# Kernel tuning notes

Measured on AMD Instinct MI355X. Metric: run time of the kernel, lower is better.

The kernel has to match this reference:

```python
import math
import jax, jax.numpy as jnp
import numpy as np

DIM = 2048
HEAD_DIM = 64
N_HEADS = DIM // HEAD_DIM
BATCH = 4
SEQ = 1025  # 32*32 axial positions + 1 zero position
EPS = 1e-6


def make_theta(head_dim=HEAD_DIM, h=32, w=32):
    # freqs: geometric from pi to 10*pi, head_dim//4 of them
    n_freqs = head_dim // 4
    freqs = jnp.exp(jnp.linspace(math.log(math.pi), math.log(10 * math.pi), n_freqs))
    hp = jnp.linspace(-1.0, 1.0, h + 1)
    wp = jnp.linspace(-1.0, 1.0, w + 1)
    hp = (hp[:-1] + hp[1:]) / 2
    wp = (wp[:-1] + wp[1:]) / 2
    pos = jnp.stack(jnp.meshgrid(hp, wp, indexing='ij'), axis=-1).reshape(h * w, 2)
    pos = jnp.concatenate([jnp.zeros((1, 2)), pos], axis=0)  # [1025, 2]
    theta_h = pos[:, 0:1] * freqs  # [S, n_freqs]
    theta_w = pos[:, 1:2] * freqs
    return jnp.concatenate([theta_h, theta_w], axis=-1)  # [S, head_dim//2]


def rms_norm(x, scale, eps=EPS):
    mean_sq = jnp.mean(jnp.square(x.astype(jnp.float32)), axis=-1, keepdims=True)
    s = scale.astype(jnp.float32) * jax.lax.rsqrt(mean_sq + eps)
    return (x * s.astype(x.dtype)).astype(x.dtype)


def apply_rotary(x, theta):
    # x: [B, H, S, D], theta: [S, d] with 2*d <= D
    d = theta.shape[-1]
    x1, x2, x3 = x[..., :d], x[..., d:2 * d], x[..., 2 * d:]
    cos, sin = jnp.cos(theta), jnp.sin(theta)  # broadcast over B, H
    y1 = x1 * cos - x2 * sin
    y2 = x2 * cos + x1 * sin
    return jnp.concatenate([y1, y2, x3], axis=-1)


def setup_inputs() -> dict:
    key = jax.random.key(0)
    k1, k2, k3 = jax.random.split(key, 3)
    x = jax.random.normal(k1, (BATCH, SEQ, DIM), dtype=jnp.float32)
    scale = jnp.ones((DIM,), dtype=jnp.float32)
    w_qkv = jax.random.normal(k2, (3 * DIM, DIM), dtype=jnp.float32) * 0.02
    w_out = jax.random.normal(k3, (DIM, DIM), dtype=jnp.float32) * 0.02
    return {"x": x, "scale": scale, "w_qkv": w_qkv, "w_out": w_out}


def reference(x, scale, w_qkv, w_out):
    B, S, _ = x.shape
    skip = x
    h = rms_norm(x, scale)
    qkv = h @ w_qkv.T  # [B, S, 3*DIM]
    qkv = qkv.reshape(B, S, 3, N_HEADS, HEAD_DIM)
    qkv = jnp.transpose(qkv, (0, 3, 2, 1, 4))  # [B, H, 3, S, D]
    q, k, v = qkv[:, :, 0], qkv[:, :, 1], qkv[:, :, 2]
    theta = make_theta()[:S]
    q = apply_rotary(q, theta)
    k = apply_rotary(k, theta)
    scores = jnp.einsum('bhqd,bhkd->bhqk', q, k) / math.sqrt(HEAD_DIM)
    causal = jnp.tril(jnp.ones((S, S), dtype=bool))
    scores = jnp.where(causal, scores, jnp.finfo(scores.dtype).min)
    attn = jax.nn.softmax(scores, axis=-1)
    o = jnp.einsum('bhqk,bhkd->bhqd', attn, v)  # [B, H, S, D]
    o = jnp.transpose(o, (0, 2, 1, 3)).reshape(B, S, DIM)
    return o @ w_out.T + skip
```

## Files before the change

kernel.cpp:

```cpp
#include <hip/hip_runtime.h>
#include <hip/hip_bf16.h>
#include <cstdint>

#define SEQ   1025
#define SPAD  1088
#define DIM   2048
#define NQKV  6144
#define MROWS 4100
#define MPAD  4224
#define NH    32

typedef __attribute__((ext_vector_type(8))) short bf16x8;
typedef __attribute__((ext_vector_type(4))) short bf16x4;
typedef __attribute__((ext_vector_type(4))) float f32x4;

#define MFMA16x16(A,B,C) __builtin_amdgcn_mfma_f32_16x16x32_bf16(A,B,C,0,0,0)

static __device__ __forceinline__ float bf2f(short s) {
    union { unsigned int u; float f; } v;
    v.u = ((unsigned int)(unsigned short)s) << 16;
    return v.f;
}
static __device__ __forceinline__ short f2bf(float f) {
    union { float f; unsigned int u; } v; v.f = f;
    unsigned int r = v.u + 0x7fffu + ((v.u >> 16) & 1u);
    return (short)(r >> 16);
}

typedef __attribute__((address_space(1))) unsigned int u32g;
typedef __attribute__((address_space(3))) unsigned int u32l;
static __device__ __forceinline__ void gld_lds16(void* lds, const void* g) {
    __builtin_amdgcn_global_load_lds((const u32g*)(uintptr_t)g,
                                     (u32l*)(uintptr_t)lds, 16, 0, 0);
}

__global__ __launch_bounds__(256) void trig_k(float* __restrict__ cosT, float* __restrict__ sinT) {
    int i = blockIdx.x * 256 + threadIdx.x;
    if (i >= SEQ * 16) return;
    int s = i >> 4, f = i & 15;
    float ph = 0.f, pw = 0.f;
    if (s > 0) {
        int p = s - 1;
        ph = -1.f + ((p >> 5) + 0.5f) * 0.0625f;
        pw = -1.f + ((p & 31) + 0.5f) * 0.0625f;
    }
    double fr = 3.141592653589793 * exp((double)f * 0.15350567286626973);
    float th = (float)(ph * fr), tw = (float)(pw * fr);
    cosT[s*32 + f]      = cosf(th);
    sinT[s*32 + f]      = sinf(th);
    cosT[s*32 + 16 + f] = cosf(tw);
    sinT[s*32 + 16 + f] = sinf(tw);
}

__global__ __launch_bounds__(256) void rmsnorm_k(const float* __restrict__ x,
                                                 const float* __restrict__ sc,
                                                 short* __restrict__ h) {
    int row = blockIdx.x, t = threadIdx.x;
    short* hr = h + (size_t)row * DIM;
    if (row >= MROWS) {
        bf16x8 z = {};
        *(bf16x8*)(hr + t*8) = z;
        return;
    }
    const float4* xr = (const float4*)(x + (size_t)row * DIM);
    float4 a = xr[2*t], b = xr[2*t+1];
    float ss = a.x*a.x + a.y*a.y + a.z*a.z + a.w*a.w
             + b.x*b.x + b.y*b.y + b.z*b.z + b.w*b.w;
    #pragma unroll
    for (int off = 32; off; off >>= 1) ss += __shfl_xor(ss, off, 64);
    __shared__ float red[4];
    if ((t & 63) == 0) red[t >> 6] = ss;
    __syncthreads();
    float ms = (red[0]+red[1]+red[2]+red[3]) * (1.0f/2048.0f);
    float inv = rsqrtf(ms + 1e-6f);
    const float4* sr = (const float4*)sc;
    float4 s0 = sr[2*t], s1 = sr[2*t+1];
    bf16x8 o;
    o[0]=f2bf(a.x*(s0.x*inv)); o[1]=f2bf(a.y*(s0.y*inv));
    o[2]=f2bf(a.z*(s0.z*inv)); o[3]=f2bf(a.w*(s0.w*inv));
    o[4]=f2bf(b.x*(s1.x*inv)); o[5]=f2bf(b.y*(s1.y*inv));
    o[6]=f2bf(b.z*(s1.z*inv)); o[7]=f2bf(b.w*(s1.w*inv));
    *(bf16x8*)(hr + t*8) = o;
}

__global__ __launch_bounds__(256) void conv_k(const float* __restrict__ in, short* __restrict__ o, int n4) {
    int i = blockIdx.x * 256 + threadIdx.x;
    if (i >= n4) return;
    float4 v = ((const float4*)in)[i];
    bf16x4 r = { f2bf(v.x), f2bf(v.y), f2bf(v.z), f2bf(v.w) };
    *(bf16x4*)(o + (size_t)i*4) = r;
}

template<int WRITE_BF16>
__global__ __launch_bounds__(256) void gemm_bt(const short* __restrict__ A,
                                               const short* __restrict__ B,
                                               void* __restrict__ C,
                                               const float* __restrict__ skip,
                                               int N, int K) {
    __shared__ short As[128*32];
    __shared__ short Bs[128*32];
    const int bm = blockIdx.x, bn = blockIdx.y;
    const int t = threadIdx.x;
    const int w = t >> 6, l = t & 63;
    const int lr = l & 15, lg = l >> 4;
    const int wr = w >> 1, wc = w & 1;
    const short* Ab = A + (size_t)bm * 128 * K;
    const short* Bb = B + (size_t)bn * 128 * K;

    f32x4 acc[4][4] = {};

    const int c1 = t + 256;
    const int ar0 = t >> 2,  ac0 = (t & 3) * 8;
    const int ar1 = c1 >> 2, ac1 = (c1 & 3) * 8;

    for (int k0 = 0; k0 < K; k0 += 32) {
        gld_lds16((char*)As + (w << 10),        Ab + (size_t)ar0 * K + k0 + ac0);
        gld_lds16((char*)As + 4096 + (w << 10), Ab + (size_t)ar1 * K + k0 + ac1);
        gld_lds16((char*)Bs + (w << 10),        Bb + (size_t)ar0 * K + k0 + ac0);
        gld_lds16((char*)Bs + 4096 + (w << 10), Bb + (size_t)ar1 * K + k0 + ac1);
        __syncthreads();
        bf16x8 af[4], bfv[4];
        #pragma unroll
        for (int m = 0; m < 4; ++m)
            af[m] = *(const bf16x8*)(As + (wr*64 + m*16 + lr)*32 + lg*8);
        #pragma unroll
        for (int n = 0; n < 4; ++n)
            bfv[n] = *(const bf16x8*)(Bs + (wc*64 + n*16 + lr)*32 + lg*8);
        #pragma unroll
        for (int m = 0; m < 4; ++m)
            #pragma unroll
            for (int n = 0; n < 4; ++n)
                acc[m][n] = MFMA16x16(af[m], bfv[n], acc[m][n]);
        __syncthreads();
    }

    #pragma unroll
    for (int m = 0; m < 4; ++m) {
        const int row0 = bm*128 + wr*64 + m*16 + lg*4;
        #pragma unroll
        for (int n = 0; n < 4; ++n) {
            const int col = bn*128 + wc*64 + n*16 + lr;
            #pragma unroll
            for (int r = 0; r < 4; ++r) {
                const int row = row0 + r;
                if constexpr (WRITE_BF16) {
                    ((short*)C)[(size_t)row * N + col] = f2bf(acc[m][n][r]);
                } else {
                    if (row < MROWS)
                        ((float*)C)[(size_t)row * N + col] =
                            acc[m][n][r] + skip[(size_t)row * N + col];
                }
            }
        }
    }
}

__global__ __launch_bounds__(256) void rearrange_k(const short* __restrict__ qkv,
        const float* __restrict__ cosT, const float* __restrict__ sinT,
        short* __restrict__ kr, short* __restrict__ vt) {
    int bid = blockIdx.x;
    int bh = bid / 17, st = bid % 17;
    int b = bh >> 5, hh = bh & 31;
    int s0 = st * 64;
    int t = threadIdx.x;
    __shared__ short vs[64][68];
    #pragma unroll
    for (int i = 0; i < 8; ++i) {
        int task = t + i*256;
        int sl = task >> 5, p = task & 31;
        int s = s0 + sl;
        float y1 = 0.f, y2 = 0.f;
        if (s < SEQ) {
            const short* src = qkv + (size_t)(b*SEQ + s)*NQKV + DIM + hh*64;
            float x1 = bf2f(src[p]), x2 = bf2f(src[32+p]);
            float c = cosT[s*32+p], sn = sinT[s*32+p];
            y1 = x1*c - x2*sn;
            y2 = x2*c + x1*sn;
        }
        short* dst = kr + ((size_t)bh*SPAD + s)*64;
        dst[p]    = f2bf(y1);
        dst[32+p] = f2bf(y2);
    }
    #pragma unroll
    for (int i = 0; i < 16; ++i) {
        int task = t + i*256;
        int sl = task >> 6, d = task & 63;
        int s = s0 + sl;
        short v = 0;
        if (s < SEQ) v = qkv[(size_t)(b*SEQ + s)*NQKV + 2*DIM + hh*64 + d];
        vs[sl][d] = v;
    }
    __syncthreads();
    #pragma unroll
    for (int i = 0; i < 16; ++i) {
        int task = t + i*256;
        int d = task >> 6, sl = task & 63;
        vt[((size_t)bh*64 + d)*SPAD + s0 + sl] = vs[sl][d];
    }
}

__global__ __launch_bounds__(256) void attn_k(const short* __restrict__ qkv,
        const short* __restrict__ kr, const short* __restrict__ vt,
        const float* __restrict__ cosT, const float* __restrict__ sinT,
        short* __restrict__ ob) {
    const int bh = blockIdx.y;
    const int b = bh >> 5, hh = bh & 31;
    const int q0 = blockIdx.x * 64;
    const int t = threadIdx.x, w = t >> 6, l = t & 63;
    const int lr = l & 15, lg = l >> 4;

    __shared__ short Ks[32*64];
    __shared__ short Vts[64*32];

    const int qrow = q0 + w*16 + lr;
    const int qc = qrow < SEQ ? qrow : SEQ-1;
    const short* qsrc = qkv + (size_t)(b*SEQ + qc)*NQKV + hh*64;
    bf16x8 xlo = *(const bf16x8*)(qsrc + lg*8);
    bf16x8 xhi = *(const bf16x8*)(qsrc + 32 + lg*8);
    const float4* cp = (const float4*)(cosT + qc*32 + lg*8);
    const float4* sp = (const float4*)(sinT + qc*32 + lg*8);
    float cc[8], sn[8];
    { float4 u = cp[0], v2 = cp[1];
      cc[0]=u.x; cc[1]=u.y; cc[2]=u.z; cc[3]=u.w;
      cc[4]=v2.x; cc[5]=v2.y; cc[6]=v2.z; cc[7]=v2.w; }
    { float4 u = sp[0], v2 = sp[1];
      sn[0]=u.x; sn[1]=u.y; sn[2]=u.z; sn[3]=u.w;
      sn[4]=v2.x; sn[5]=v2.y; sn[6]=v2.z; sn[7]=v2.w; }
    bf16x8 qf0, qf1;
    #pragma unroll
    for (int j = 0; j < 8; ++j) {
        float x1 = bf2f(xlo[j]), x2 = bf2f(xhi[j]);
        qf0[j] = f2bf(x1*cc[j] - x2*sn[j]);
        qf1[j] = f2bf(x2*cc[j] + x1*sn[j]);
    }

    f32x4 oacc[4] = {};
    float mrun = -1e30f, lrun = 0.f;
    const int ntile = min((q0 + 64 + 31) >> 5, 33);
    const float SC = 0.125f * 1.4426950408889634f;

    const short* kbase = kr + (size_t)bh * SPAD * 64;
    const short* vbase = vt + (size_t)bh * 64 * SPAD;

    const int skrow = t >> 3, skslot = t & 7;
    const int svrow = t >> 2, svslot = t & 3;

    for (int kt = 0; kt < ntile; ++kt) {
        const int kv0 = kt * 32;
        gld_lds16((char*)Ks + (w<<10),
                  (const char*)(kbase + (size_t)(kv0 + skrow)*64) + ((skslot ^ (skrow & 7)) << 4));
        gld_lds16((char*)Vts + (w<<10),
                  (const char*)(vbase + (size_t)svrow*SPAD + kv0) + ((svslot ^ ((svrow>>1) & 3)) << 4));
        __syncthreads();

        f32x4 st0 = {}, st1 = {};
        {
            const int krow = lr;
            const int swz = (krow & 7) << 4;
            const char* kp = (const char*)Ks + krow*128;
            bf16x8 a0 = *(const bf16x8*)(kp + ((lg*16) ^ swz));
            bf16x8 a1 = *(const bf16x8*)(kp + ((64 + lg*16) ^ swz));
            st0 = MFMA16x16(a0, qf0, st0);
            st0 = MFMA16x16(a1, qf1, st0);
        }
        {
            const int krow = 16 + lr;
            const int swz = (krow & 7) << 4;
            const char* kp = (const char*)Ks + krow*128;
            bf16x8 a0 = *(const bf16x8*)(kp + ((lg*16) ^ swz));
            bf16x8 a1 = *(const bf16x8*)(kp + ((64 + lg*16) ^ swz));
            st1 = MFMA16x16(a0, qf0, st1);
            st1 = MFMA16x16(a1, qf1, st1);
        }

        float sv[8];
        float tmax = -1e30f;
        #pragma unroll
        for (int r = 0; r < 4; ++r) {
            int kv = kv0 + lg*4 + r;
            float v = st0[r] * SC;
            v = (kv <= qrow && kv < SEQ) ? v : -1e30f;
            sv[r] = v; tmax = fmaxf(tmax, v);
        }
        #pragma unroll
        for (int r = 0; r < 4; ++r) {
            int kv = kv0 + 16 + lg*4 + r;
            float v = st1[r] * SC;
            v = (kv <= qrow && kv < SEQ) ? v : -1e30f;
            sv[4+r] = v; tmax = fmaxf(tmax, v);
        }
        tmax = fmaxf(tmax, __shfl_xor(tmax, 16, 64));
        tmax = fmaxf(tmax, __shfl_xor(tmax, 32, 64));
        float mnew = fmaxf(mrun, tmax);
        float alpha = exp2f(mrun - mnew);
        float psum = 0.f;
        bf16x8 pf;
        #pragma unroll
        for (int i2 = 0; i2 < 8; ++i2) {
            float p = exp2f(sv[i2] - mnew);
            psum += p;
            pf[i2] = f2bf(p);
        }
        psum += __shfl_xor(psum, 16, 64);
        psum += __shfl_xor(psum, 32, 64);
        lrun = lrun * alpha + psum;
        mrun = mnew;
        #pragma unroll
        for (int df = 0; df < 4; ++df) {
            oacc[df][0] *= alpha; oacc[df][1] *= alpha;
            oacc[df][2] *= alpha; oacc[df][3] *= alpha;
        }
        #pragma unroll
        for (int df = 0; df < 4; ++df) {
            const int vrow = df*16 + lr;
            const int swz = ((vrow >> 1) & 3) << 4;
            const char* vp = (const char*)Vts + vrow*64;
            bf16x4 v0 = *(const bf16x4*)(vp + ((lg*8) ^ swz));
            bf16x4 v1 = *(const bf16x4*)(vp + ((32 + lg*8) ^ swz));
            bf16x8 vf;
            vf[0]=v0[0]; vf[1]=v0[1]; vf[2]=v0[2]; vf[3]=v0[3];
            vf[4]=v1[0]; vf[5]=v1[1]; vf[6]=v1[2]; vf[7]=v1[3];
            oacc[df] = MFMA16x16(vf, pf, oacc[df]);
        }
        __syncthreads();
    }

    if (qrow < SEQ) {
        float inv = 1.0f / lrun;
        short* orow = ob + (size_t)(b*SEQ + qrow)*DIM + hh*64;
        #pragma unroll
        for (int df = 0; df < 4; ++df) {
            bf16x4 ov = { f2bf(oacc[df][0]*inv), f2bf(oacc[df][1]*inv),
                          f2bf(oacc[df][2]*inv), f2bf(oacc[df][3]*inv) };
            *(bf16x4*)(orow + df*16 + lg*4) = ov;
        }
    }
}

extern "C" void kernel_launch(void* const* d_in, const int* in_sizes, int n_in,
                              void* d_out, int out_size, void* d_ws, size_t ws_size,
                              hipStream_t stream) {
    const float* x     = (const float*)d_in[0];
    const float* scale = (const float*)d_in[1];
    const float* w_qkv = (const float*)d_in[2];
    const float* w_out = (const float*)d_in[3];
    float* out = (float*)d_out;

    char* ws = (char*)d_ws;
    size_t off = 0;
    auto alloc = [&](size_t bytes) -> char* {
        char* p = ws + off;
        off += (bytes + 255) & ~(size_t)255;
        return p;
    };
    float* cosT  = (float*)alloc((size_t)SEQ*32*4);
    float* sinT  = (float*)alloc((size_t)SEQ*32*4);
    short* h_b   = (short*)alloc((size_t)MPAD*DIM*2);
    short* wq_b  = (short*)alloc((size_t)NQKV*DIM*2);
    short* wo_b  = (short*)alloc((size_t)DIM*DIM*2);
    short* qkv_b = (short*)alloc((size_t)MPAD*NQKV*2);
    short* k_r   = (short*)alloc((size_t)128*SPAD*64*2);
    short* vt    = (short*)alloc((size_t)128*SPAD*64*2);
    short* o_b   = h_b;

    trig_k<<<65, 256, 0, stream>>>(cosT, sinT);
    rmsnorm_k<<<MPAD, 256, 0, stream>>>(x, scale, h_b);
    conv_k<<<(NQKV*DIM/4 + 255)/256, 256, 0, stream>>>(w_qkv, wq_b, NQKV*DIM/4);
    conv_k<<<(DIM*DIM/4 + 255)/256, 256, 0, stream>>>(w_out, wo_b, DIM*DIM/4);
    gemm_bt<1><<<dim3(33,48), 256, 0, stream>>>(h_b, wq_b, qkv_b, nullptr, NQKV, DIM);
    rearrange_k<<<128*17, 256, 0, stream>>>(qkv_b, cosT, sinT, k_r, vt);
    attn_k<<<dim3(17,128), 256, 0, stream>>>(qkv_b, k_r, vt, cosT, sinT, o_b);
    gemm_bt<0><<<dim3(33,16), 256, 0, stream>>>(o_b, wo_b, out, x, DIM, DIM);
}
```

Before: 504.4 us.

## Add 256x256 8-wave pipelined QKV GEMM with XCD-aware block remapping

Replaces the 128x128 QKV projection GEMM with a new 512-thread kernel that uses 256x256 tiles, a double-buffered LDS stage fed by global-to-LDS loads, XOR-swizzled LDS layout, and explicit barrier/priority scheduling to overlap loads with MFMA work. Row padding grows to a multiple of 256 to fit the bigger tile. The attention and output GEMM launches switch to 1D grids with a block-id remap that groups consecutive tiles per XCD for better L2 locality. The large tiles raise data reuse but use 128KB of LDS and more registers, and the padding adds a little wasted compute.

```diff
diff --git a/kernel.cpp b/kernel.cpp
--- a/kernel.cpp
+++ b/kernel.cpp
@@ -7,7 +7,7 @@
 #define DIM   2048
 #define NQKV  6144
 #define MROWS 4100
-#define MPAD  4224
+#define MPAD  4352
 #define NH    32
 
 typedef __attribute__((ext_vector_type(8))) short bf16x8;
@@ -33,6 +33,9 @@
     __builtin_amdgcn_global_load_lds((const u32g*)(uintptr_t)g,
                                      (u32l*)(uintptr_t)lds, 16, 0, 0);
 }
+
+#define SBX() __builtin_amdgcn_sched_barrier(0)
+#define PRIO(x) __builtin_amdgcn_s_setprio(x)
 
 __global__ __launch_bounds__(256) void trig_k(float* __restrict__ cosT, float* __restrict__ sinT) {
     int i = blockIdx.x * 256 + threadIdx.x;
@@ -91,15 +94,141 @@
     *(bf16x4*)(o + (size_t)i*4) = r;
 }
 
-template<int WRITE_BF16>
+__global__ __launch_bounds__(512, 2) void gemm8p(const short* __restrict__ A,
+                                                 const short* __restrict__ B,
+                                                 short* __restrict__ C,
+                                                 int N, int K, int nbm) {
+    extern __shared__ char smem[];
+    const int nwg = gridDim.x;
+    const int cpx = nwg >> 3;
+    const int bid = blockIdx.x;
+    const int sid = (bid & 7) * cpx + (bid >> 3);
+    const int bm = sid % nbm;
+    const int bn = sid / nbm;
+
+    const int t = threadIdx.x, w = t >> 6, l = t & 63;
+    const int lr = l & 15, lg = l >> 4;
+    const int wr = w >> 2, wc = w & 3;
+
+    const short* Ab = A + (size_t)bm * 256 * K;
+    const short* Bb = B + (size_t)bn * 256 * K;
+
+    const int srow = t >> 3;
+    const int scol = (((t & 7) ^ (srow & 7)) << 3);
+
+    const int cs0 = (lg * 16) ^ ((lr & 7) << 4);
+    const int cs1 = (64 + lg * 16) ^ ((lr & 7) << 4);
+    const int aRowB = (wr * 128 + lr) * 128;
+    const int bRowB = (wc * 64 + lr) * 128;
+
+    f32x4 acc[8][4] = {};
+    bf16x8 rA[4][2], rB[4][2];
+
+#define STAGE8(kt, bb) do {                                                   \
+    const int k0_ = (kt) * 64;                                                \
+    _Pragma("unroll")                                                         \
+    for (int c = 0; c < 4; ++c) {                                             \
+        gld_lds16(smem + (bb)*65536 + c*8192 + (w<<10),                       \
+                  Ab + (size_t)(c*64 + srow) * K + k0_ + scol);               \
+        gld_lds16(smem + (bb)*65536 + 32768 + c*8192 + (w<<10),               \
+                  Bb + (size_t)(c*64 + srow) * K + k0_ + scol);               \
+    }                                                                         \
+} while (0)
+
+#define READ_A8(bb, h) do {                                                   \
+    const char* p_ = smem + (bb)*65536 + aRowB + (h)*8192;                    \
+    _Pragma("unroll")                                                         \
+    for (int am = 0; am < 4; ++am) {                                          \
+        rA[am][0] = *(const bf16x8*)(p_ + am*2048 + cs0);                     \
+        rA[am][1] = *(const bf16x8*)(p_ + am*2048 + cs1);                     \
+    }                                                                         \
+} while (0)
+
+#define READ_B4(bb, np) do {                                                  \
+    const char* p_ = smem + (bb)*65536 + 32768 + bRowB + (np)*4096;           \
+    _Pragma("unroll")                                                         \
+    for (int nn = 0; nn < 2; ++nn) {                                          \
+        rB[(np)*2+nn][0] = *(const bf16x8*)(p_ + nn*2048 + cs0);              \
+        rB[(np)*2+nn][1] = *(const bf16x8*)(p_ + nn*2048 + cs1);              \
+    }                                                                         \
+} while (0)
+
+#define MF_Q(h, nh) do {                                                      \
+    _Pragma("unroll")                                                         \
+    for (int am = 0; am < 4; ++am)                                            \
+    _Pragma("unroll")                                                         \
+    for (int nn = 0; nn < 2; ++nn) {                                          \
+        acc[(h)*4+am][(nh)*2+nn] =                                            \
+            MFMA16x16(rA[am][0], rB[(nh)*2+nn][0], acc[(h)*4+am][(nh)*2+nn]); \
+        acc[(h)*4+am][(nh)*2+nn] =                                            \
+            MFMA16x16(rA[am][1], rB[(nh)*2+nn][1], acc[(h)*4+am][(nh)*2+nn]); \
+    }                                                                         \
+} while (0)
+
+#define PH_COMPUTE(h, nh) do {                                                \
+    SBX(); __builtin_amdgcn_s_barrier();                                      \
+    asm volatile("s_waitcnt lgkmcnt(0)" ::: "memory"); SBX();                 \
+    PRIO(1); MF_Q(h, nh); PRIO(0); SBX();                                     \
+    __builtin_amdgcn_s_barrier(); SBX();                                      \
+} while (0)
+
+    STAGE8(0, 0);
+    STAGE8(1, 1);
+    asm volatile("s_waitcnt vmcnt(8)" ::: "memory"); SBX();
+    __builtin_amdgcn_s_barrier(); SBX();
+
+    const int NT2 = K / 128;
+    for (int it = 0; it < NT2; ++it) {
+        const bool more = (it < NT2 - 1);
+        READ_A8(0, 0); READ_B4(0, 0); PH_COMPUTE(0, 0);
+        READ_B4(0, 1);                PH_COMPUTE(0, 1);
+        READ_A8(0, 1);                PH_COMPUTE(1, 1);
+        if (more) STAGE8(2*it + 2, 0);
+        SBX(); __builtin_amdgcn_s_barrier(); SBX();
+        PRIO(1); MF_Q(1, 0); PRIO(0); SBX();
+        if (more) { asm volatile("s_waitcnt vmcnt(8)" ::: "memory"); }
+        else      { asm volatile("s_waitcnt vmcnt(0)" ::: "memory"); }
+        SBX(); __builtin_amdgcn_s_barrier(); SBX();
+        READ_A8(1, 0); READ_B4(1, 0); PH_COMPUTE(0, 0);
+        READ_B4(1, 1);                PH_COMPUTE(0, 1);
+        READ_A8(1, 1);                PH_COMPUTE(1, 1);
+        if (more) STAGE8(2*it + 3, 1);
+        SBX(); __builtin_amdgcn_s_barrier(); SBX();
+        PRIO(1); MF_Q(1, 0); PRIO(0); SBX();
+        if (more) { asm volatile("s_waitcnt vmcnt(8)" ::: "memory"); SBX(); }
+        __builtin_amdgcn_s_barrier(); SBX();
+    }
+
+    #pragma unroll
+    for (int m = 0; m < 8; ++m) {
+        const int row0 = bm*256 + wr*128 + m*16 + lg*4;
+        #pragma unroll
+        for (int n = 0; n < 4; ++n) {
+            const int col = bn*256 + wc*64 + n*16 + lr;
+            #pragma unroll
+            for (int r = 0; r < 4; ++r)
+                C[(size_t)(row0 + r) * N + col] = f2bf(acc[m][n][r]);
+        }
+    }
+#undef STAGE8
+#undef READ_A8
+#undef READ_B4
+#undef MF_Q
+#undef PH_COMPUTE
+}
+
 __global__ __launch_bounds__(256) void gemm_bt(const short* __restrict__ A,
                                                const short* __restrict__ B,
-                                               void* __restrict__ C,
+                                               float* __restrict__ C,
                                                const float* __restrict__ skip,
-                                               int N, int K) {
+                                               int N, int K, int nbm) {
     __shared__ short As[128*32];
     __shared__ short Bs[128*32];
-    const int bm = blockIdx.x, bn = blockIdx.y;
+    const int nwg = gridDim.x;
+    const int cpx = nwg >> 3;
+    const int bid = blockIdx.x;
+    const int sid = (bid & 7) * cpx + (bid >> 3);
+    const int bm = sid % nbm, bn = sid / nbm;
     const int t = threadIdx.x;
     const int w = t >> 6, l = t & 63;
     const int lr = l & 15, lg = l >> 4;
@@ -143,13 +272,9 @@
             #pragma unroll
             for (int r = 0; r < 4; ++r) {
                 const int row = row0 + r;
-                if constexpr (WRITE_BF16) {
-                    ((short*)C)[(size_t)row * N + col] = f2bf(acc[m][n][r]);
-                } else {
-                    if (row < MROWS)
-                        ((float*)C)[(size_t)row * N + col] =
-                            acc[m][n][r] + skip[(size_t)row * N + col];
-                }
+                if (row < MROWS)
+                    C[(size_t)row * N + col] =
+                        acc[m][n][r] + skip[(size_t)row * N + col];
             }
         }
     }
@@ -203,9 +328,13 @@
         const short* __restrict__ kr, const short* __restrict__ vt,
         const float* __restrict__ cosT, const float* __restrict__ sinT,
         short* __restrict__ ob) {
-    const int bh = blockIdx.y;
+    const int nwg = gridDim.x;
+    const int cpx = nwg >> 3;
+    const int bid = blockIdx.x;
+    const int sid = (bid & 7) * cpx + (bid >> 3);
+    const int bh = sid / 17;
+    const int q0 = (sid % 17) * 64;
     const int b = bh >> 5, hh = bh & 31;
-    const int q0 = blockIdx.x * 64;
     const int t = threadIdx.x, w = t >> 6, l = t & 63;
     const int lr = l & 15, lg = l >> 4;
 
@@ -363,12 +492,15 @@
     short* vt    = (short*)alloc((size_t)128*SPAD*64*2);
     short* o_b   = h_b;
 
+    hipFuncSetAttribute((const void*)gemm8p,
+                        hipFuncAttributeMaxDynamicSharedMemorySize, 131072);
+
     trig_k<<<65, 256, 0, stream>>>(cosT, sinT);
     rmsnorm_k<<<MPAD, 256, 0, stream>>>(x, scale, h_b);
     conv_k<<<(NQKV*DIM/4 + 255)/256, 256, 0, stream>>>(w_qkv, wq_b, NQKV*DIM/4);
     conv_k<<<(DIM*DIM/4 + 255)/256, 256, 0, stream>>>(w_out, wo_b, DIM*DIM/4);
-    gemm_bt<1><<<dim3(33,48), 256, 0, stream>>>(h_b, wq_b, qkv_b, nullptr, NQKV, DIM);
+    gemm8p<<<(MPAD/256)*(NQKV/256), 512, 131072, stream>>>(h_b, wq_b, qkv_b, NQKV, DIM, MPAD/256);
     rearrange_k<<<128*17, 256, 0, stream>>>(qkv_b, cosT, sinT, k_r, vt);
-    attn_k<<<dim3(17,128), 256, 0, stream>>>(qkv_b, k_r, vt, cosT, sinT, o_b);
-    gemm_bt<0><<<dim3(33,16), 256, 0, stream>>>(o_b, wo_b, out, x, DIM, DIM);
-}
+    attn_k<<<17*128, 256, 0, stream>>>(qkv_b, k_r, vt, cosT, sinT, o_b);
+    gemm_bt<<<(MPAD/128)*(DIM/128), 256, 0, stream>>>(o_b, wo_b, out, x, DIM, DIM, MPAD/128);
+}
```

Measured after the change: 467.2 us. -7.4%, faster.
